# Performance work log

Hardware: AMD Instinct MI355X
Metric: run time of the kernel (lower is better)

Reference implementation:

```python
import jax, jax.numpy as jnp
import numpy as np

LN_EPS = 1e-5

def _mha(xq, xkv, in_w, in_b, out_w, out_b, n_heads):
    # torch nn.MultiheadAttention, batch_first=True, dropout=0
    B, S, d = xq.shape
    T = xkv.shape[1]
    dh = d // n_heads
    wq, wk, wv = jnp.split(in_w, 3, axis=0)   # each [d, d]
    bq, bk, bv = jnp.split(in_b, 3)
    q = (xq @ wq.T + bq).reshape(B, S, n_heads, dh).transpose(0, 2, 1, 3)
    k = (xkv @ wk.T + bk).reshape(B, T, n_heads, dh).transpose(0, 2, 1, 3)
    v = (xkv @ wv.T + bv).reshape(B, T, n_heads, dh).transpose(0, 2, 1, 3)
    scores = jnp.einsum('bhsd,bhtd->bhst', q, k) / jnp.sqrt(jnp.asarray(dh, xq.dtype))
    attn = jax.nn.softmax(scores, axis=-1)    # explicit [B,H,S,T] weights (need_weights=True path)
    o = jnp.einsum('bhst,bhtd->bhsd', attn, v)
    o = o.transpose(0, 2, 1, 3).reshape(B, S, d)
    return o @ out_w.T + out_b

def _ln(x, g, b):
    mu = jnp.mean(x, axis=-1, keepdims=True)
    var = jnp.mean(jnp.square(x - mu), axis=-1, keepdims=True)
    return (x - mu) / jnp.sqrt(var + LN_EPS) * g + b

def setup_inputs() -> dict:
    key = jax.random.key(0)
    B, S, T, d, ff = 4, 1024, 1024, 1024, 4096
    ks = jax.random.split(key, 10)
    s = 0.02
    return {
        'x': jax.random.normal(ks[0], (B, S, d), jnp.float32),
        'mem': jax.random.normal(ks[1], (B, T, d), jnp.float32),
        'sa_in_w': jax.random.normal(ks[2], (3 * d, d), jnp.float32) * s,
        'sa_in_b': jnp.zeros((3 * d,), jnp.float32),
        'sa_out_w': jax.random.normal(ks[3], (d, d), jnp.float32) * s,
        'sa_out_b': jnp.zeros((d,), jnp.float32),
        'ca_in_w': jax.random.normal(ks[4], (3 * d, d), jnp.float32) * s,
        'ca_in_b': jnp.zeros((3 * d,), jnp.float32),
        'ca_out_w': jax.random.normal(ks[5], (d, d), jnp.float32) * s,
        'ca_out_b': jnp.zeros((d,), jnp.float32),
        'ff_w1': jax.random.normal(ks[6], (ff, d), jnp.float32) * s,
        'ff_b1': jnp.zeros((ff,), jnp.float32),
        'ff_w2': jax.random.normal(ks[7], (d, ff), jnp.float32) * s,
        'ff_b2': jnp.zeros((d,), jnp.float32),
        'ln1_g': jnp.ones((d,), jnp.float32), 'ln1_b': jnp.zeros((d,), jnp.float32),
        'ln2_g': jnp.ones((d,), jnp.float32), 'ln2_b': jnp.zeros((d,), jnp.float32),
        'ln3_g': jnp.ones((d,), jnp.float32), 'ln3_b': jnp.zeros((d,), jnp.float32),
        'n_heads': 16,
    }

def reference(x, mem, sa_in_w, sa_in_b, sa_out_w, sa_out_b,
              ca_in_w, ca_in_b, ca_out_w, ca_out_b,
              ff_w1, ff_b1, ff_w2, ff_b2,
              ln1_g, ln1_b, ln2_g, ln2_b, ln3_g, ln3_b, n_heads):
    sa = _mha(x, x, sa_in_w, sa_in_b, sa_out_w, sa_out_b, n_heads)
    x = _ln(x + sa, ln1_g, ln1_b)
    ca = _mha(x, mem, ca_in_w, ca_in_b, ca_out_w, ca_out_b, n_heads)
    x = _ln(x + ca, ln2_g, ln2_b)
    h = jax.nn.gelu(x @ ff_w1.T + ff_b1, approximate=False)  # torch nn.GELU default = exact erf
    ff = h @ ff_w2.T + ff_b2
    return _ln(x + ff, ln3_g, ln3_b)
```

## Files before the change

kernel.cpp:

```cpp
#include <hip/hip_runtime.h>
#include <cstddef>

#define D_MODEL 1024
#define SEQ     1024
#define BATCH   4
#define NHEAD   16
#define DH      64
#define FFDIM   4096
#define NTOK    (BATCH*SEQ)

typedef float f32x4  __attribute__((ext_vector_type(4)));
typedef short bf16x8 __attribute__((ext_vector_type(8)));

static __device__ __forceinline__ unsigned short f2bf(float x){
  union { float f; unsigned u; } v; v.f = x;
  unsigned r = v.u + 0x7fffu + ((v.u >> 16) & 1u);
  return (unsigned short)(r >> 16);
}

static __device__ __forceinline__ unsigned short f2bf_t(float x){
  union { float f; unsigned u; } v; v.f = x;
  return (unsigned short)(v.u >> 16);
}

static __device__ __forceinline__ float bf2f(unsigned short h){
  union { unsigned u; float f; } v; v.u = ((unsigned)h) << 16; return v.f;
}

static __device__ __forceinline__ float fast_exp2(float x){
#if __has_builtin(__builtin_amdgcn_exp2f)
  return __builtin_amdgcn_exp2f(x);
#else
  return __expf(x * 0.69314718056f);
#endif
}

static __device__ __forceinline__ void gl_lds16(const void* g, void* l){
  __builtin_amdgcn_global_load_lds((const __attribute__((address_space(1))) void*)g,
                                   (__attribute__((address_space(3))) void*)l, 16, 0, 0);
}

#define WAITV(n) asm volatile("s_waitcnt vmcnt(" #n ")" ::: "memory")
#define WAITL0() asm volatile("s_waitcnt lgkmcnt(0)" ::: "memory")
#define SBAR()   __builtin_amdgcn_s_barrier()
#define SCHED0() __builtin_amdgcn_sched_barrier(0)

static __device__ __forceinline__ int2 swz_tile(int gx, int RX, int RY){
  int id = blockIdx.y * gx + blockIdx.x;
  int x = id & 7, s = id >> 3;
  int nrx = gx / RX;
  int bx = (x % nrx) * RX + (s % RX);
  int by = (x / nrx) * RY + (s / RX);
  return make_int2(bx, by);
}

struct CvtJobs {
  const float* src[8];
  unsigned short* dst[8];
  int n[8];
};

__global__ __launch_bounds__(256) void cvt_kernel(CvtJobs jobs){
  int seg = blockIdx.y;
  const float* s = jobs.src[seg];
  unsigned short* d = jobs.dst[seg];
  int n = jobs.n[seg];
  int stride = gridDim.x * 256 * 4;
  for (int i = (blockIdx.x*256 + threadIdx.x)*4; i < n; i += stride){
    float4 v = *(const float4*)(s + i);
    ushort4 o;
    o.x = f2bf(v.x); o.y = f2bf(v.y); o.z = f2bf(v.z); o.w = f2bf(v.w);
    *(ushort4*)(d + i) = o;
  }
}

static __device__ __forceinline__ int cidx(int row, int col){
  return row*128 + (((col >> 3) ^ (row & 15)) << 3) + (col & 7);
}

template<int EPI>
static __device__ __forceinline__ void gemm_core(
    unsigned short* smem,
    const unsigned short* __restrict__ A,
    const unsigned short* __restrict__ B,
    const float* __restrict__ bias,
    void* __restrict__ out0,
    unsigned short* __restrict__ vt,
    int N, int K, int kbeg, int kend, int row0, int col0,
    int split, int ldout)
{
  unsigned short* As = smem;
  unsigned short* Bs = smem + 128*64;
  const int tid  = threadIdx.x;
  const int w    = tid >> 6, lane = tid & 63;
  const int quad = lane >> 4, l15 = lane & 15;
  const int lr   = lane >> 3, lc = lane & 7;
  const int csrc = lc ^ lr;
  const int sw   = l15 & 7;
  const int wm = (w >> 1) * 64, wn = (w & 1) * 64;

  f32x4 acc[4][4];
  const f32x4 zero4 = {0.f, 0.f, 0.f, 0.f};
  #pragma unroll
  for (int i=0;i<4;i++)
    #pragma unroll
    for (int j=0;j<4;j++)
      acc[i][j] = zero4;

  const unsigned short* Ag = A + (size_t)(row0 + lr)*K + csrc*8;
  const unsigned short* Bg = B + (size_t)(col0 + lr)*K + csrc*8;

  for (int k0 = kbeg; k0 < kend; k0 += 64){
    #pragma unroll
    for (int i=0;i<4;i++){
      gl_lds16(Ag + (size_t)(i*32 + w*8)*K + k0, &As[i*2048 + w*512]);
      gl_lds16(Bg + (size_t)(i*32 + w*8)*K + k0, &Bs[i*2048 + w*512]);
    }
    __syncthreads();
    #pragma unroll
    for (int ks=0; ks<2; ks++){
      bf16x8 af[4], bfr[4];
      #pragma unroll
      for (int i=0;i<4;i++)
        af[i] = *(const bf16x8*)&As[(wm + i*16 + l15)*64 + ((ks*4 + quad) ^ sw)*8];
      #pragma unroll
      for (int j=0;j<4;j++)
        bfr[j] = *(const bf16x8*)&Bs[(wn + j*16 + l15)*64 + ((ks*4 + quad) ^ sw)*8];
      #pragma unroll
      for (int i=0;i<4;i++)
        #pragma unroll
        for (int j=0;j<4;j++)
          acc[i][j] = __builtin_amdgcn_mfma_f32_16x16x32_bf16(af[i], bfr[j], acc[i][j], 0, 0, 0);
    }
    __syncthreads();
  }

  float bj[4];
  #pragma unroll
  for (int j=0;j<4;j++) bj[j] = bias[col0 + wn + j*16 + l15];

  unsigned short* Cs = smem;

  #pragma unroll
  for (int i=0;i<4;i++){
    #pragma unroll
    for (int r=0;r<4;r++){
      int lrow = wm + i*16 + quad*4 + r;
      #pragma unroll
      for (int j=0;j<4;j++){
        int lcol = wn + j*16 + l15;
        float v = acc[i][j][r] + bj[j];
        Cs[cidx(lrow, lcol)] = f2bf(v);
      }
    }
  }
  __syncthreads();

  const int ld = N;
  #pragma unroll
  for (int p=0;p<2;p++){
    int c = p*64 + (tid >> 2);
    unsigned short* dst = (unsigned short*)out0 + (size_t)(row0 + c)*ld + col0;
    #pragma unroll
    for (int k=0;k<4;k++){
      int m = (tid & 3) + k*4;
      bf16x8 val = *(const bf16x8*)&Cs[c*128 + ((m ^ (c & 15)) << 3)];
      *(bf16x8*)(dst + m*8) = val;
    }
  }
}

__global__ __launch_bounds__(256) void gemm_split(
    const unsigned short* A, const unsigned short* B, const float* bias,
    unsigned short* outA, unsigned short* outB, int N, int K)
{
  __shared__ __align__(16) unsigned short smem[2*128*64];
  int2 t = swz_tile(gridDim.x, 4, 8);
  int kseg = K >> 1;
  int kbeg = blockIdx.z * kseg;
  unsigned short* o = blockIdx.z ? outB : outA;
  gemm_core<1>(smem, A, B, bias, o, nullptr, N, K, kbeg, kbeg + kseg,
               t.y*128, t.x*128, 0, 0);
}

#define G256_STAGE(k0, dstp) do{                                              \
    unsigned short* _d = (dstp);                                              \
    const int _k = (k0);                                                      \
    gl_lds16(Ag + (size_t)(0*64 + w*8)*K + _k, _d + 0*4096 + w*512);          \
    gl_lds16(Ag + (size_t)(1*64 + w*8)*K + _k, _d + 1*4096 + w*512);          \
    gl_lds16(Ag + (size_t)(2*64 + w*8)*K + _k, _d + 2*4096 + w*512);          \
    gl_lds16(Ag + (size_t)(3*64 + w*8)*K + _k, _d + 3*4096 + w*512);          \
    gl_lds16(Bg + (size_t)(0*64 + w*8)*K + _k, _d + 16384 + 0*4096 + w*512);  \
    gl_lds16(Bg + (size_t)(1*64 + w*8)*K + _k, _d + 16384 + 1*4096 + w*512);  \
    gl_lds16(Bg + (size_t)(2*64 + w*8)*K + _k, _d + 16384 + 2*4096 + w*512);  \
    gl_lds16(Bg + (size_t)(3*64 + w*8)*K + _k, _d + 16384 + 3*4096 + w*512);  \
  }while(0)

#define G256_CMP(bufp) do{                                                    \
    const unsigned short* As_ = (bufp);                                       \
    const unsigned short* Bs_ = (bufp) + 16384;                               \
    _Pragma("unroll")                                                         \
    for (int ks=0; ks<2; ks++){                                               \
      const int ch = ((ks*4 + quad) ^ sw)*8;                                  \
      bf16x8 bfr[4], af[4];                                                   \
      _Pragma("unroll")                                                       \
      for (int j=0;j<4;j++)                                                   \
        bfr[j] = *(const bf16x8*)&Bs_[(wc*64 + j*16 + l15)*64 + ch];          \
      _Pragma("unroll")                                                       \
      for (int i=0;i<4;i++)                                                   \
        af[i] = *(const bf16x8*)&As_[(wr*128 + i*16 + l15)*64 + ch];          \
      __builtin_amdgcn_s_setprio(1);                                          \
      _Pragma("unroll")                                                       \
      for (int i=0;i<4;i++)                                                   \
        _Pragma("unroll")                                                     \
        for (int j=0;j<4;j++)                                                 \
          acc[i][j] = __builtin_amdgcn_mfma_f32_16x16x32_bf16(af[i], bfr[j], acc[i][j], 0, 0, 0); \
      __builtin_amdgcn_s_setprio(0);                                          \
      _Pragma("unroll")                                                       \
      for (int i=0;i<4;i++)                                                   \
        af[i] = *(const bf16x8*)&As_[(wr*128 + (i+4)*16 + l15)*64 + ch];      \
      __builtin_amdgcn_s_setprio(1);                                          \
      _Pragma("unroll")                                                       \
      for (int i=0;i<4;i++)                                                   \
        _Pragma("unroll")                                                     \
        for (int j=0;j<4;j++)                                                 \
          acc[i+4][j] = __builtin_amdgcn_mfma_f32_16x16x32_bf16(af[i], bfr[j], acc[i+4][j], 0, 0, 0); \
      __builtin_amdgcn_s_setprio(0);                                          \
    }                                                                         \
  }while(0)

template<int EPI>
static __device__ __forceinline__ void gemm256_core(
    unsigned short* smem,
    const unsigned short* __restrict__ A,
    const unsigned short* __restrict__ B,
    const float* __restrict__ bias,
    void* __restrict__ out0,
    unsigned short* __restrict__ vt,
    int N, int K, int kbeg, int kend, int row0, int col0,
    int split, int ldout)
{
  const int tid  = threadIdx.x;
  const int w    = tid >> 6, lane = tid & 63;
  const int quad = lane >> 4, l15 = lane & 15;
  const int lr   = lane >> 3, lc = lane & 7;
  const int csrc = lc ^ lr;
  const int sw   = l15 & 7;
  const int wr   = w >> 2, wc = w & 3;

  f32x4 acc[8][4];
  const f32x4 zero4 = {0.f, 0.f, 0.f, 0.f};
  #pragma unroll
  for (int i=0;i<8;i++)
    #pragma unroll
    for (int j=0;j<4;j++)
      acc[i][j] = zero4;

  const unsigned short* Ag = A + (size_t)(row0 + lr)*K + csrc*8;
  const unsigned short* Bg = B + (size_t)(col0 + lr)*K + csrc*8;

  unsigned short* buf0 = smem;
  unsigned short* buf1 = smem + 32768;

  G256_STAGE(kbeg,      buf0);
  G256_STAGE(kbeg + 64, buf1);
  WAITV(8); SBAR(); SCHED0();

  for (int t=0; t<8; t++){
    const int kb = kbeg + t*128;
    G256_CMP(buf0);
    WAITL0(); SCHED0();
    SBAR();
    if (t < 7){ G256_STAGE(kb + 128, buf0); WAITV(8); }
    else      { WAITV(0); }
    SBAR(); SCHED0();
    G256_CMP(buf1);
    WAITL0(); SCHED0();
    SBAR();
    if (t < 7){ G256_STAGE(kb + 192, buf1); WAITV(8); }
    SBAR(); SCHED0();
  }

  float bj[4];
  #pragma unroll
  for (int j=0;j<4;j++) bj[j] = bias[col0 + wc*64 + j*16 + l15];

  const bool vtile = (EPI == 5) && (col0 >= split);
  unsigned short* Cs = smem;

  #pragma unroll
  for (int i=0;i<8;i++){
    #pragma unroll
    for (int r=0;r<4;r++){
      int lrow = wr*128 + i*16 + quad*4 + r;
      #pragma unroll
      for (int j=0;j<4;j++){
        int lcol = wc*64 + j*16 + l15;
        float v = acc[i][j][r] + bj[j];
        if (EPI == 2){
          float t = 0.7978845608f * (v + 0.044715f * v * v * v);
          float e = __expf(2.f * t);
          float th = 1.f - 2.f * __builtin_amdgcn_rcpf(e + 1.f);
          v = 0.5f * v * (1.f + th);
        }
        int rr = vtile ? lcol : lrow, cc = vtile ? lrow : lcol;
        Cs[rr*256 + (((cc >> 3) ^ (rr & 31)) << 3) + (cc & 7)] = f2bf(v);
      }
    }
  }
  __syncthreads();

  const int ld = (EPI == 5) ? ldout : N;
  #pragma unroll
  for (int p=0;p<2;p++){
    int c = p*128 + (tid >> 2);
    unsigned short* dst;
    if (!vtile){
      dst = (unsigned short*)out0 + (size_t)(row0 + c)*ld + col0;
    } else {
      int colg = (col0 - split) + c;
      int hh = colg >> 6, dd = colg & 63;
      int bb = row0 >> 10, t0 = row0 & 1023;
      dst = vt + ((size_t)(bb*NHEAD + hh)*DH + dd)*SEQ + t0;
    }
    #pragma unroll
    for (int k=0;k<8;k++){
      int m = (tid & 3) + k*4;
      bf16x8 val = *(const bf16x8*)&Cs[c*256 + ((m ^ (c & 31)) << 3)];
      *(bf16x8*)(dst + m*8) = val;
    }
  }
}

__global__ __launch_bounds__(512, 2) void gemm256_ffn1(
    const unsigned short* A, const unsigned short* B, const float* bias,
    unsigned short* out0, int N, int K)
{
  __shared__ __align__(16) unsigned short smem[2*2*256*64];
  int2 t = swz_tile(gridDim.x, 4, 8);
  gemm256_core<2>(smem, A, B, bias, out0, nullptr, N, K, 0, K,
                  t.y*256, t.x*256, 0, 0);
}

__global__ __launch_bounds__(512, 2) void gemm_kv256(
    const unsigned short* xb, const unsigned short* memb,
    const unsigned short* wsa, const unsigned short* wca,
    const float* bsa, const float* bca,
    unsigned short* ksa, unsigned short* vtsa,
    unsigned short* kca, unsigned short* vtca)
{
  __shared__ __align__(16) unsigned short smem[2*2*256*64];
  const int id = blockIdx.x;
  const int xcd = id & 7, s = id >> 3;
  const bool sa = s < 16;
  const int u = sa ? s : s - 16;
  const int bx = (xcd & 3)*2 + (u & 1);
  const int by = (xcd >> 2)*8 + (u >> 1);
  gemm256_core<5>(smem, sa ? xb : memb, sa ? wsa : wca, sa ? bsa : bca,
                  sa ? ksa : kca, sa ? vtsa : vtca,
                  2048, 1024, 0, 1024, by*256, bx*256, 1024, 1024);
}

__global__ __launch_bounds__(512, 2) void gemm256_split4(
    const unsigned short* A, const unsigned short* B, const float* bias,
    unsigned short* o0, unsigned short* o1, unsigned short* o2, unsigned short* o3,
    int N, int K)
{
  __shared__ __align__(16) unsigned short smem[2*2*256*64];
  const int id = blockIdx.x;
  const int xcd = id & 7, s = id >> 3;
  const int z  = xcd >> 1;
  const int bx = s & 3;
  const int by = (xcd & 1)*8 + (s >> 2);
  const int kseg = K >> 2, kbeg = z * kseg;
  unsigned short* o = (z == 0) ? o0 : (z == 1) ? o1 : (z == 2) ? o2 : o3;
  gemm256_core<1>(smem, A, B, bias, o, nullptr, N, K, kbeg, kbeg + kseg,
                  by*256, bx*256, 0, 0);
}

__global__ __launch_bounds__(256) void attn_kernel(
    const unsigned short* __restrict__ Xa,
    const unsigned short* __restrict__ Wq,
    const float* __restrict__ bq,
    const unsigned short* __restrict__ Kp,
    const unsigned short* __restrict__ Vt,
    unsigned short* __restrict__ O)
{
  __shared__ __align__(16) unsigned short Ks[64*64];
  __shared__ __align__(16) unsigned short Vs[64*64];
  __shared__ __align__(16) unsigned short Bu[4*16*72];

  const int tid  = threadIdx.x;
  const int w    = tid >> 6, lane = tid & 63;
  const int quad = lane >> 4, l15 = lane & 15;
  const int lr   = lane >> 3, lc = lane & 7;
  const int csrc = lc ^ lr;
  const int sw   = l15 & 7;
  const int id = blockIdx.x;
  const int xc = id & 7, s = id >> 3;
  const int bh = xc*8 + (s >> 4), qt = s & 15;
  const int b = bh >> 4, h = bh & 15;
  const int q0   = qt * 64;
  const int tok0 = b * SEQ;
  const int hoff = h * DH;

  const f32x4 zero4 = {0.f, 0.f, 0.f, 0.f};

  f32x4 qacc[4];
  #pragma unroll
  for (int dj=0;dj<4;dj++) qacc[dj] = zero4;

  const unsigned short* Ag = Xa + (size_t)(tok0 + q0 + lr)*1024 + csrc*8;
  const unsigned short* Wg = Wq + (size_t)(hoff + lr)*1024 + csrc*8;

  for (int k0 = 0; k0 < 1024; k0 += 64){
    #pragma unroll
    for (int i=0;i<2;i++)
      gl_lds16(Ag + (size_t)(i*32 + w*8)*1024 + k0, &Bu[i*2048 + w*512]);
    #pragma unroll
    for (int i=0;i<2;i++)
      gl_lds16(Wg + (size_t)(i*32 + w*8)*1024 + k0, &Ks[i*2048 + w*512]);
    __syncthreads();
    #pragma unroll
    for (int ks=0; ks<2; ks++){
      const int ch = ((ks*4 + quad) ^ sw)*8;
      bf16x8 af = *(const bf16x8*)&Bu[(w*16 + l15)*64 + ch];
      bf16x8 bfr[4];
      #pragma unroll
      for (int dj=0;dj<4;dj++)
        bfr[dj] = *(const bf16x8*)&Ks[(dj*16 + l15)*64 + ch];
      #pragma unroll
      for (int dj=0;dj<4;dj++)
        qacc[dj] = __builtin_amdgcn_mfma_f32_16x16x32_bf16(af, bfr[dj], qacc[dj], 0, 0, 0);
    }
    __syncthreads();
  }

  {
    const float QSCALE = 0.125f * 1.44269504f;
    float biasv[4];
    #pragma unroll
    for (int dj=0;dj<4;dj++) biasv[dj] = bq[hoff + dj*16 + l15];
    #pragma unroll
    for (int dj=0;dj<4;dj++)
      #pragma unroll
      for (int r=0;r<4;r++){
        int q = w*16 + quad*4 + r;
        int d = dj*16 + l15;
        Bu[q*64 + (((d>>3) ^ (q&7))<<3) + (d&7)] = f2bf((qacc[dj][r] + biasv[dj]) * QSCALE);
      }
  }
  __syncthreads();

  bf16x8 qb[2];
  {
    int row = w*16 + l15;
    qb[0] = *(const bf16x8*)&Bu[row*64 + ((0 + quad) ^ sw)*8];
    qb[1] = *(const bf16x8*)&Bu[row*64 + ((4 + quad) ^ sw)*8];
  }

  float lsum = 0.f;
  f32x4 oacc[4];
  #pragma unroll
  for (int dt=0;dt<4;dt++) oacc[dt] = zero4;

  unsigned short* pw = &Bu[w*16*72];

  for (int kc = 0; kc < SEQ/64; ++kc){
    __syncthreads();
    #pragma unroll
    for (int i=0;i<2;i++){
      int r = i*32 + w*8 + lr;
      gl_lds16(Kp + (size_t)(tok0 + kc*64 + r)*1024 + hoff + csrc*8, &Ks[i*2048 + w*512]);
      gl_lds16(Vt + ((size_t)bh*DH + r)*SEQ + kc*64 + csrc*8,        &Vs[i*2048 + w*512]);
    }
    __syncthreads();

    #pragma unroll
    for (int tj=0;tj<4;tj++){
      bf16x8 ka0 = *(const bf16x8*)&Ks[(tj*16 + l15)*64 + ((0 + quad) ^ sw)*8];
      bf16x8 ka1 = *(const bf16x8*)&Ks[(tj*16 + l15)*64 + ((4 + quad) ^ sw)*8];
      f32x4 z = zero4;
      __builtin_amdgcn_s_setprio(1);
      z = __builtin_amdgcn_mfma_f32_16x16x32_bf16(ka0, qb[0], z, 0, 0, 0);
      z = __builtin_amdgcn_mfma_f32_16x16x32_bf16(ka1, qb[1], z, 0, 0, 0);
      __builtin_amdgcn_s_setprio(0);
      float p0 = fast_exp2(z[0]);
      float p1 = fast_exp2(z[1]);
      float p2 = fast_exp2(z[2]);
      float p3 = fast_exp2(z[3]);
      lsum += (p0 + p1) + (p2 + p3);
      short4 pk;
      pk.x = (short)f2bf_t(p0); pk.y = (short)f2bf_t(p1);
      pk.z = (short)f2bf_t(p2); pk.w = (short)f2bf_t(p3);
      *(short4*)&pw[l15*72 + tj*16 + quad*4] = pk;
    }

    __builtin_amdgcn_s_setprio(1);
    {
      bf16x8 pa0 = *(const bf16x8*)&pw[l15*72 + quad*8];
      bf16x8 pa1 = *(const bf16x8*)&pw[l15*72 + 32 + quad*8];
      #pragma unroll
      for (int dt=0;dt<4;dt++){
        bf16x8 vb0 = *(const bf16x8*)&Vs[(dt*16 + l15)*64 + ((0 + quad) ^ sw)*8];
        bf16x8 vb1 = *(const bf16x8*)&Vs[(dt*16 + l15)*64 + ((4 + quad) ^ sw)*8];
        oacc[dt] = __builtin_amdgcn_mfma_f32_16x16x32_bf16(pa0, vb0, oacc[dt], 0, 0, 0);
        oacc[dt] = __builtin_amdgcn_mfma_f32_16x16x32_bf16(pa1, vb1, oacc[dt], 0, 0, 0);
      }
    }
    __builtin_amdgcn_s_setprio(0);
  }

  lsum += __shfl_xor(lsum, 16);
  lsum += __shfl_xor(lsum, 32);

  __syncthreads();
  unsigned short* OB = Bu;
  #pragma unroll
  for (int r=0;r<4;r++){
    float lv = __shfl(lsum, quad*4 + r);
    float rinv = __builtin_amdgcn_rcpf(lv);
    int q = w*16 + quad*4 + r;
    #pragma unroll
    for (int dt=0;dt<4;dt++){
      int d = dt*16 + l15;
      OB[q*64 + (((d>>3) ^ (q&7))<<3) + (d&7)] = f2bf(oacc[dt][r] * rinv);
    }
  }
  __syncthreads();
  {
    int q = tid >> 2;
    unsigned short* dst = O + (size_t)(tok0 + q0 + q)*D_MODEL + hoff;
    #pragma unroll
    for (int k=0;k<2;k++){
      int m = (tid & 3) + k*4;
      bf16x8 val = *(const bf16x8*)&OB[q*64 + ((m ^ (q & 7)) << 3)];
      *(bf16x8*)(dst + m*8) = val;
    }
  }
}

__global__ __launch_bounds__(256) void ln_kernel(
    const float* __restrict__ resid,
    const unsigned short* __restrict__ d1,
    const unsigned short* __restrict__ d2,
    const unsigned short* __restrict__ d3,
    const unsigned short* __restrict__ d4,
    const float* __restrict__ g, const float* __restrict__ beta,
    float* __restrict__ outf, unsigned short* __restrict__ outb)
{
  const int row = blockIdx.x;
  const int t = threadIdx.x;
  const size_t base = (size_t)row * D_MODEL;
  float4 a = *(const float4*)(resid + base + t*4);
  ushort4 p4 = *(const ushort4*)(d1 + base + t*4);
  ushort4 q4 = *(const ushort4*)(d2 + base + t*4);
  float v0 = a.x + bf2f(p4.x) + bf2f(q4.x);
  float v1 = a.y + bf2f(p4.y) + bf2f(q4.y);
  float v2 = a.z + bf2f(p4.z) + bf2f(q4.z);
  float v3 = a.w + bf2f(p4.w) + bf2f(q4.w);
  if (d3){
    ushort4 r4 = *(const ushort4*)(d3 + base + t*4);
    ushort4 s4 = *(const ushort4*)(d4 + base + t*4);
    v0 += bf2f(r4.x) + bf2f(s4.x);
    v1 += bf2f(r4.y) + bf2f(s4.y);
    v2 += bf2f(r4.z) + bf2f(s4.z);
    v3 += bf2f(r4.w) + bf2f(s4.w);
  }
  float s1 = v0+v1+v2+v3;
  float s2 = v0*v0+v1*v1+v2*v2+v3*v3;
  #pragma unroll
  for (int off=32; off>0; off>>=1){
    s1 += __shfl_down(s1, off);
    s2 += __shfl_down(s2, off);
  }
  __shared__ float red[8];
  const int wid = t >> 6;
  if ((t & 63) == 0){ red[wid*2] = s1; red[wid*2+1] = s2; }
  __syncthreads();
  s1 = red[0]+red[2]+red[4]+red[6];
  s2 = red[1]+red[3]+red[5]+red[7];
  float mean = s1 * (1.f/1024.f);
  float var  = s2 * (1.f/1024.f) - mean*mean;
  float rstd = rsqrtf(var + 1e-5f);
  float4 gg = *(const float4*)(g + t*4);
  float4 bb = *(const float4*)(beta + t*4);
  float y0 = (v0-mean)*rstd*gg.x + bb.x;
  float y1 = (v1-mean)*rstd*gg.y + bb.y;
  float y2 = (v2-mean)*rstd*gg.z + bb.z;
  float y3 = (v3-mean)*rstd*gg.w + bb.w;
  if (outf) *(float4*)(outf + base + t*4) = make_float4(y0,y1,y2,y3);
  if (outb){
    ushort4 o;
    o.x = f2bf(y0); o.y = f2bf(y1); o.z = f2bf(y2); o.w = f2bf(y3);
    *(ushort4*)(outb + base + t*4) = o;
  }
}

extern "C" void kernel_launch(void* const* d_in, const int* in_sizes, int n_in,
                              void* d_out, int out_size, void* d_ws, size_t ws_size,
                              hipStream_t stream)
{
  const float* x        = (const float*)d_in[0];
  const float* mem      = (const float*)d_in[1];
  const float* sa_in_w  = (const float*)d_in[2];
  const float* sa_in_b  = (const float*)d_in[3];
  const float* sa_out_w = (const float*)d_in[4];
  const float* sa_out_b = (const float*)d_in[5];
  const float* ca_in_w  = (const float*)d_in[6];
  const float* ca_in_b  = (const float*)d_in[7];
  const float* ca_out_w = (const float*)d_in[8];
  const float* ca_out_b = (const float*)d_in[9];
  const float* ff_w1    = (const float*)d_in[10];
  const float* ff_b1    = (const float*)d_in[11];
  const float* ff_w2    = (const float*)d_in[12];
  const float* ff_b2    = (const float*)d_in[13];
  const float* ln1_g    = (const float*)d_in[14];
  const float* ln1_b    = (const float*)d_in[15];
  const float* ln2_g    = (const float*)d_in[16];
  const float* ln2_b    = (const float*)d_in[17];
  const float* ln3_g    = (const float*)d_in[18];
  const float* ln3_b    = (const float*)d_in[19];

  char* base = (char*)d_ws;
  size_t off = 0;
  auto alloc = [&](size_t bytes) -> void* {
    void* r = base + off;
    off += (bytes + 255) & ~(size_t)255;
    return r;
  };
  unsigned short* xb     = (unsigned short*)alloc((size_t)NTOK*1024*2);
  unsigned short* memb   = (unsigned short*)alloc((size_t)NTOK*1024*2);
  unsigned short* wsain  = (unsigned short*)alloc((size_t)3072*1024*2);
  unsigned short* wsaout = (unsigned short*)alloc((size_t)1024*1024*2);
  unsigned short* wcain  = (unsigned short*)alloc((size_t)3072*1024*2);
  unsigned short* wcaout = (unsigned short*)alloc((size_t)1024*1024*2);
  unsigned short* wff1   = (unsigned short*)alloc((size_t)4096*1024*2);
  unsigned short* wff2   = (unsigned short*)alloc((size_t)4096*1024*2);
  unsigned short* qkvbuf = (unsigned short*)alloc((size_t)NTOK*3072*2);
  unsigned short* attnb  = (unsigned short*)alloc((size_t)NTOK*1024*2);
  float*          proj   = (float*)alloc((size_t)NTOK*1024*4);
  float*          x1f    = (float*)alloc((size_t)NTOK*1024*4);
  unsigned short* x1b    = (unsigned short*)alloc((size_t)NTOK*1024*2);
  float*          x2f    = (float*)alloc((size_t)NTOK*1024*4);
  unsigned short* x2b    = (unsigned short*)alloc((size_t)NTOK*1024*2);

  unsigned short* ksa  = qkvbuf;
  unsigned short* vtsa = qkvbuf + (size_t)NTOK*1024;
  unsigned short* kca  = qkvbuf + (size_t)NTOK*2048;
  unsigned short* vtca = (unsigned short*)x2f;
  unsigned short* hbuf = qkvbuf;
  unsigned short* pA   = (unsigned short*)proj;
  unsigned short* pB   = (unsigned short*)xb;
  unsigned short* q0p  = (unsigned short*)proj;
  unsigned short* q1p  = (unsigned short*)proj + (size_t)NTOK*1024;
  unsigned short* q2p  = (unsigned short*)x1f;
  unsigned short* q3p  = (unsigned short*)x1f + (size_t)NTOK*1024;

  CvtJobs jobs;
  jobs.src[0]=x;        jobs.dst[0]=xb;     jobs.n[0]=NTOK*1024;
  jobs.src[1]=mem;      jobs.dst[1]=memb;   jobs.n[1]=NTOK*1024;
  jobs.src[2]=sa_in_w;  jobs.dst[2]=wsain;  jobs.n[2]=3072*1024;
  jobs.src[3]=sa_out_w; jobs.dst[3]=wsaout; jobs.n[3]=1024*1024;
  jobs.src[4]=ca_in_w;  jobs.dst[4]=wcain;  jobs.n[4]=3072*1024;
  jobs.src[5]=ca_out_w; jobs.dst[5]=wcaout; jobs.n[5]=1024*1024;
  jobs.src[6]=ff_w1;    jobs.dst[6]=wff1;   jobs.n[6]=4096*1024;
  jobs.src[7]=ff_w2;    jobs.dst[7]=wff2;   jobs.n[7]=4096*1024;
  cvt_kernel<<<dim3(1024,8), 256, 0, stream>>>(jobs);

  gemm_kv256<<<256, 512, 0, stream>>>(xb, memb,
                                      wsain + (size_t)1024*1024, wcain + (size_t)1024*1024,
                                      sa_in_b + 1024, ca_in_b + 1024,
                                      ksa, vtsa, kca, vtca);

  attn_kernel<<<1024, 256, 0, stream>>>(xb, wsain, sa_in_b, ksa, vtsa, attnb);
  gemm_split<<<dim3(8,32,2), 256, 0, stream>>>(attnb, wsaout, sa_out_b, pA, pB, 1024, 1024);
  ln_kernel<<<NTOK, 256, 0, stream>>>(x, pA, pB, nullptr, nullptr, ln1_g, ln1_b, x1f, x1b);

  attn_kernel<<<1024, 256, 0, stream>>>(x1b, wcain, ca_in_b, kca, vtca, attnb);
  gemm_split<<<dim3(8,32,2), 256, 0, stream>>>(attnb, wcaout, ca_out_b, pA, pB, 1024, 1024);
  ln_kernel<<<NTOK, 256, 0, stream>>>(x1f, pA, pB, nullptr, nullptr, ln2_g, ln2_b, x2f, x2b);

  gemm256_ffn1<<<dim3(16,16), 512, 0, stream>>>(x2b, wff1, ff_b1, hbuf, 4096, 1024);
  gemm256_split4<<<256, 512, 0, stream>>>(hbuf, wff2, ff_b2, q0p, q1p, q2p, q3p, 1024, 4096);
  ln_kernel<<<NTOK, 256, 0, stream>>>(x2f, q0p, q1p, q2p, q3p, ln3_g, ln3_b, (float*)d_out, nullptr);
}
```

Before: 434.0 us.

## Interleave split global-to-LDS staging with MFMA phases in 256-tile GEMM

The 256-row GEMM main loop is restructured from two big compute/stage halves per iteration into 16 iterations, each split into four MFMA phases of two A row-blocks apiece. Global-to-LDS loads for the B tile and two halves of the A tile are issued between these phases, partly into the buffer currently being consumed once its parts are no longer read. The aim is to overlap memory traffic with matrix math more finely and reduce the stalls at barriers. The cost is more barriers per k-step and fragile wait-count and buffer-reuse ordering, which could cause races if miscounted.

```diff
diff --git a/kernel.cpp b/kernel.cpp
--- a/kernel.cpp
+++ b/kernel.cpp
@@ -183,50 +183,53 @@
                t.y*128, t.x*128, 0, 0);
 }
 
-#define G256_STAGE(k0, dstp) do{                                              \
-    unsigned short* _d = (dstp);                                              \
-    const int _k = (k0);                                                      \
-    gl_lds16(Ag + (size_t)(0*64 + w*8)*K + _k, _d + 0*4096 + w*512);          \
-    gl_lds16(Ag + (size_t)(1*64 + w*8)*K + _k, _d + 1*4096 + w*512);          \
-    gl_lds16(Ag + (size_t)(2*64 + w*8)*K + _k, _d + 2*4096 + w*512);          \
-    gl_lds16(Ag + (size_t)(3*64 + w*8)*K + _k, _d + 3*4096 + w*512);          \
+#define G256_LDB(bufp) do{                                                    \
+    const unsigned short* Bs_ = (bufp) + 16384;                               \
+    _Pragma("unroll")                                                         \
+    for (int ks=0; ks<2; ks++){                                               \
+      const int ch = ((ks*4 + quad) ^ sw)*8;                                  \
+      _Pragma("unroll")                                                       \
+      for (int j=0;j<4;j++)                                                   \
+        bfr[ks][j] = *(const bf16x8*)&Bs_[(wc*64 + j*16 + l15)*64 + ch];      \
+    }                                                                         \
+  }while(0)
+
+#define G256_LDA(bufp, S) do{                                                 \
+    const unsigned short* As_ = (bufp);                                       \
+    _Pragma("unroll")                                                         \
+    for (int ks=0; ks<2; ks++){                                               \
+      const int ch = ((ks*4 + quad) ^ sw)*8;                                  \
+      afr[ks][0] = *(const bf16x8*)&As_[(wr*128 + (2*(S)  )*16 + l15)*64 + ch]; \
+      afr[ks][1] = *(const bf16x8*)&As_[(wr*128 + (2*(S)+1)*16 + l15)*64 + ch]; \
+    }                                                                         \
+  }while(0)
+
+#define G256_PH(S) do{                                                        \
+    __builtin_amdgcn_s_setprio(1);                                            \
+    _Pragma("unroll")                                                         \
+    for (int ks=0; ks<2; ks++){                                               \
+      _Pragma("unroll")                                                       \
+      for (int j=0;j<4;j++){                                                  \
+        acc[2*(S)  ][j] = __builtin_amdgcn_mfma_f32_16x16x32_bf16(afr[ks][0], bfr[ks][j], acc[2*(S)  ][j], 0, 0, 0); \
+        acc[2*(S)+1][j] = __builtin_amdgcn_mfma_f32_16x16x32_bf16(afr[ks][1], bfr[ks][j], acc[2*(S)+1][j], 0, 0, 0); \
+      }                                                                       \
+    }                                                                         \
+    __builtin_amdgcn_s_setprio(0);                                            \
+  }while(0)
+
+#define STG_B4(k0, dstp) do{ unsigned short* _d=(dstp); const int _k=(k0);    \
     gl_lds16(Bg + (size_t)(0*64 + w*8)*K + _k, _d + 16384 + 0*4096 + w*512);  \
     gl_lds16(Bg + (size_t)(1*64 + w*8)*K + _k, _d + 16384 + 1*4096 + w*512);  \
     gl_lds16(Bg + (size_t)(2*64 + w*8)*K + _k, _d + 16384 + 2*4096 + w*512);  \
     gl_lds16(Bg + (size_t)(3*64 + w*8)*K + _k, _d + 16384 + 3*4096 + w*512);  \
   }while(0)
-
-#define G256_CMP(bufp) do{                                                    \
-    const unsigned short* As_ = (bufp);                                       \
-    const unsigned short* Bs_ = (bufp) + 16384;                               \
-    _Pragma("unroll")                                                         \
-    for (int ks=0; ks<2; ks++){                                               \
-      const int ch = ((ks*4 + quad) ^ sw)*8;                                  \
-      bf16x8 bfr[4], af[4];                                                   \
-      _Pragma("unroll")                                                       \
-      for (int j=0;j<4;j++)                                                   \
-        bfr[j] = *(const bf16x8*)&Bs_[(wc*64 + j*16 + l15)*64 + ch];          \
-      _Pragma("unroll")                                                       \
-      for (int i=0;i<4;i++)                                                   \
-        af[i] = *(const bf16x8*)&As_[(wr*128 + i*16 + l15)*64 + ch];          \
-      __builtin_amdgcn_s_setprio(1);                                          \
-      _Pragma("unroll")                                                       \
-      for (int i=0;i<4;i++)                                                   \
-        _Pragma("unroll")                                                     \
-        for (int j=0;j<4;j++)                                                 \
-          acc[i][j] = __builtin_amdgcn_mfma_f32_16x16x32_bf16(af[i], bfr[j], acc[i][j], 0, 0, 0); \
-      __builtin_amdgcn_s_setprio(0);                                          \
-      _Pragma("unroll")                                                       \
-      for (int i=0;i<4;i++)                                                   \
-        af[i] = *(const bf16x8*)&As_[(wr*128 + (i+4)*16 + l15)*64 + ch];      \
-      __builtin_amdgcn_s_setprio(1);                                          \
-      _Pragma("unroll")                                                       \
-      for (int i=0;i<4;i++)                                                   \
-        _Pragma("unroll")                                                     \
-        for (int j=0;j<4;j++)                                                 \
-          acc[i+4][j] = __builtin_amdgcn_mfma_f32_16x16x32_bf16(af[i], bfr[j], acc[i+4][j], 0, 0, 0); \
-      __builtin_amdgcn_s_setprio(0);                                          \
-    }                                                                         \
+#define STG_A02(k0, dstp) do{ unsigned short* _d=(dstp); const int _k=(k0);   \
+    gl_lds16(Ag + (size_t)(0*64 + w*8)*K + _k, _d + 0*4096 + w*512);          \
+    gl_lds16(Ag + (size_t)(2*64 + w*8)*K + _k, _d + 2*4096 + w*512);          \
+  }while(0)
+#define STG_A13(k0, dstp) do{ unsigned short* _d=(dstp); const int _k=(k0);   \
+    gl_lds16(Ag + (size_t)(1*64 + w*8)*K + _k, _d + 1*4096 + w*512);          \
+    gl_lds16(Ag + (size_t)(3*64 + w*8)*K + _k, _d + 3*4096 + w*512);          \
   }while(0)
 
 template<int EPI>
@@ -256,30 +259,41 @@
     for (int j=0;j<4;j++)
       acc[i][j] = zero4;
 
+  bf16x8 bfr[2][4];
+  bf16x8 afr[2][2];
+
   const unsigned short* Ag = A + (size_t)(row0 + lr)*K + csrc*8;
   const unsigned short* Bg = B + (size_t)(col0 + lr)*K + csrc*8;
 
   unsigned short* buf0 = smem;
   unsigned short* buf1 = smem + 32768;
 
-  G256_STAGE(kbeg,      buf0);
-  G256_STAGE(kbeg + 64, buf1);
-  WAITV(8); SBAR(); SCHED0();
-
-  for (int t=0; t<8; t++){
-    const int kb = kbeg + t*128;
-    G256_CMP(buf0);
-    WAITL0(); SCHED0();
-    SBAR();
-    if (t < 7){ G256_STAGE(kb + 128, buf0); WAITV(8); }
-    else      { WAITV(0); }
+  STG_B4(kbeg, buf0); STG_A02(kbeg, buf0); STG_A13(kbeg, buf0);
+  STG_B4(kbeg + 64, buf1); STG_A02(kbeg + 64, buf1);
+
+  for (int t = 0; t < 16; t++){
+    unsigned short* cur = (t & 1) ? buf1 : buf0;
+    unsigned short* oth = (t & 1) ? buf0 : buf1;
+    const int kb = kbeg + t*64;
+    if (t < 15) { WAITV(6); } else { WAITV(0); }
     SBAR(); SCHED0();
-    G256_CMP(buf1);
-    WAITL0(); SCHED0();
-    SBAR();
-    if (t < 7){ G256_STAGE(kb + 192, buf1); WAITV(8); }
-    SBAR(); SCHED0();
-  }
+    G256_LDB(cur); G256_LDA(cur, 0);
+    if (t < 15) STG_A13(kb + 64, oth);
+    G256_PH(0);
+    WAITL0(); SBAR(); SCHED0();
+    G256_LDA(cur, 1);
+    if (t < 14) STG_B4(kb + 128, cur);
+    G256_PH(1);
+    WAITL0(); SBAR(); SCHED0();
+    G256_LDA(cur, 2);
+    if (t < 14) STG_A02(kb + 128, cur);
+    G256_PH(2);
+    WAITL0(); SBAR(); SCHED0();
+    G256_LDA(cur, 3);
+    G256_PH(3);
+    WAITL0();
+  }
+  SBAR(); SCHED0();
 
   float bj[4];
   #pragma unroll
```

Result: faster. 418.6 us (-3.5%).
